# Performance work log

Measured on AMD Instinct MI355X. Metric: run time of the kernel, lower is better.

The kernel has to match this reference:

```python
import jax, jax.numpy as jnp
import numpy as np

D_EV, D_RGB, D_FUSED, D_REASON = 128, 128, 384, 384
D_INNER, D_STATE, D_CONV, DT_RANK = 2 * D_REASON, 16, 4, (D_REASON + 15) // 16
B, L = 4, 1024
LN_EPS = 1e-5


def setup_inputs() -> dict:
    key = jax.random.key(0)
    ks = jax.random.split(key, 16)
    s = lambda k, shp, scale=0.02: jax.random.normal(k, shp, jnp.float32) * scale
    inp = {
        "ev_tok": jax.random.normal(ks[0], (B, L, D_EV), jnp.float32),
        "rgb_tok": jax.random.normal(ks[1], (B, L, D_RGB), jnp.float32),
        "W_ev": s(ks[2], (D_EV, D_FUSED // 2)), "b_ev": jnp.zeros((D_FUSED // 2,), jnp.float32),
        "W_rgb": s(ks[3], (D_RGB, D_FUSED // 2)), "b_rgb": jnp.zeros((D_FUSED // 2,), jnp.float32),
        "ln_g": jnp.ones((D_FUSED,), jnp.float32), "ln_b": jnp.zeros((D_FUSED,), jnp.float32),
        "W_proj": s(ks[4], (D_FUSED, D_REASON)), "b_proj": jnp.zeros((D_REASON,), jnp.float32),
        "W_in": s(ks[5], (D_REASON, 2 * D_INNER)),
        "conv_w": s(ks[6], (D_INNER, 1, D_CONV), 0.1), "conv_b": jnp.zeros((D_INNER,), jnp.float32),
        "W_x": s(ks[7], (D_INNER, DT_RANK + 2 * D_STATE)),
        "W_dt": s(ks[8], (DT_RANK, D_INNER), 0.1), "b_dt": s(ks[9], (D_INNER,), 0.1),
        "A_log": jnp.tile(jnp.log(jnp.arange(1, D_STATE + 1, dtype=jnp.float32)), (D_INNER, 1)),
        "D_skip": jnp.ones((D_INNER,), jnp.float32),
        "W_out": s(ks[10], (D_INNER, D_REASON)),
    }
    return inp


def _selective_scan(u, delta, A, Bm, Cm, D_skip):
    # u, delta: [B,L,d]; Bm, Cm: [B,L,n]; A: [d,n]; D_skip: [d]
    deltaA = jnp.exp(delta[..., None] * A)                       # [B,L,d,n]
    deltaBu = delta[..., None] * Bm[:, :, None, :] * u[..., None]  # [B,L,d,n]

    def step(h, inp):
        dA, dBu, C_t = inp
        h = dA * h + dBu                                         # [B,d,n]
        y = jnp.einsum('bdn,bn->bd', h, C_t)
        return h, y

    h0 = jnp.zeros((u.shape[0], A.shape[0], A.shape[1]), u.dtype)
    xs = (jnp.moveaxis(deltaA, 1, 0), jnp.moveaxis(deltaBu, 1, 0), jnp.moveaxis(Cm, 1, 0))
    _, ys = jax.lax.scan(step, h0, xs)                           # [L,B,d]
    return jnp.moveaxis(ys, 0, 1) + u * D_skip


def _mamba_block(x, W_in, conv_w, conv_b, W_x, W_dt, b_dt, A_log, D_skip, W_out):
    xr = x @ W_in                                                # [B,L,2*d_inner]
    u, res = jnp.split(xr, 2, axis=-1)
    # causal depthwise conv over time
    uc = jnp.swapaxes(u, 1, 2)                                   # [B,d_inner,L]
    uc = jax.lax.conv_general_dilated(uc, conv_w, (1,), [(D_CONV - 1, 0)],
                                      dimension_numbers=('NCH', 'OIH', 'NCH'),
                                      feature_group_count=D_INNER)
    u = jax.nn.silu(jnp.swapaxes(uc, 1, 2) + conv_b)             # [B,L,d_inner]
    x_dbl = u @ W_x                                              # [B,L,dt_rank+2n]
    dt, Bm, Cm = jnp.split(x_dbl, [DT_RANK, DT_RANK + D_STATE], axis=-1)
    delta = jax.nn.softplus(dt @ W_dt + b_dt)                    # [B,L,d_inner]
    A = -jnp.exp(A_log)                                          # [d_inner,n]
    y = _selective_scan(u, delta, A, Bm, Cm, D_skip)
    y = y * jax.nn.silu(res)
    return y @ W_out


def reference(ev_tok, rgb_tok, W_ev, b_ev, W_rgb, b_rgb, ln_g, ln_b, W_proj, b_proj,
              W_in, conv_w, conv_b, W_x, W_dt, b_dt, A_log, D_skip, W_out):
    x = jnp.concatenate([ev_tok @ W_ev + b_ev, rgb_tok @ W_rgb + b_rgb], axis=-1)
    mu = jnp.mean(x, axis=-1, keepdims=True)
    var = jnp.mean(jnp.square(x - mu), axis=-1, keepdims=True)
    x = (x - mu) * jax.lax.rsqrt(var + LN_EPS) * ln_g + ln_b
    x = x @ W_proj + b_proj                                      # [B,L,d_reason]
    return _mamba_block(x, W_in, conv_w, conv_b, W_x, W_dt, b_dt, A_log, D_skip, W_out)
```

## Files before the change

### kernel.cpp

```cpp
#include <hip/hip_runtime.h>
#include <cstddef>
#include <cstdint>

#define L_SEQ 1024
#define NCHUNK 64
#define CLEN 16

typedef __bf16 bf16x8 __attribute__((ext_vector_type(8)));
typedef float f32x4 __attribute__((ext_vector_type(4)));

__device__ __forceinline__ float silu_f(float x) {
    return x / (1.f + __expf(-x));
}
__device__ __forceinline__ float exp2_fast(float x) { return exp2f(x); }

__device__ __forceinline__ unsigned short f2bf(float x) {
    union { float f; unsigned int u; } v; v.f = x;
    unsigned int r = (v.u + 0x7fffu + ((v.u >> 16) & 1u)) >> 16;
    return (unsigned short)r;
}
__device__ __forceinline__ float bf2f(unsigned short h) {
    union { float f; unsigned int u; } v; v.u = ((unsigned int)h) << 16;
    return v.f;
}
__device__ __forceinline__ unsigned int packf(float x) {
    unsigned short h = f2bf(x);
    unsigned short l = f2bf(x - bf2f(h));
    return ((unsigned int)h << 16) | (unsigned int)l;
}
__device__ __forceinline__ float unpackf(unsigned int pk) {
    return bf2f((unsigned short)(pk >> 16)) + bf2f((unsigned short)(pk & 0xffffu));
}

template<bool APK, int EPI, int SPLITS>
__global__ __launch_bounds__(256)
void gemm_bf3(const unsigned short* __restrict__ Ahi,
              const unsigned short* __restrict__ Alo,
              const unsigned int* __restrict__ Apk, int lda,
              const unsigned short* __restrict__ Bthi,
              const unsigned short* __restrict__ Btlo,
              const float* __restrict__ bias,
              float* __restrict__ Cf, float* __restrict__ Cf2,
              unsigned short* __restrict__ Chi, unsigned short* __restrict__ Clo,
              int Ks, int Ktot, int Nw)
{
    __shared__ unsigned short As[2][128][40];
    __shared__ unsigned short Bs[2][128][40];
    const int tid = threadIdx.x;
    const int lane = tid & 63;
    const int wave = tid >> 6;
    const int wm = wave >> 1, wn = wave & 1;

    const int gx = gridDim.x;
    const int nwg = gx * gridDim.y;
    const int lin = blockIdx.y * gx + blockIdx.x;
    const int swz = ((nwg & 7) == 0) ? ((lin & 7) * (nwg >> 3) + (lin >> 3)) : lin;
    const int m0 = (swz / gx) * 128, n0 = (swz % gx) * 128;
    const int z = (SPLITS > 1) ? blockIdx.z : 0;
    const int kbeg = z * Ks;

    const int srow = tid >> 1, sko = (tid & 1) * 16;

    f32x4 acc[4][4];
    #pragma unroll
    for (int i = 0; i < 4; ++i)
        #pragma unroll
        for (int j = 0; j < 4; ++j) {
            f32x4 zz = {0.f, 0.f, 0.f, 0.f};
            acc[i][j] = zz;
        }

    const size_t aoff = (size_t)(m0 + srow) * lda + sko;
    const size_t boff = (size_t)(n0 + srow) * Ktot + sko;

    uint4 ra[4], rb[4];

    auto load_regs = [&](int k0) {
        if constexpr (APK) {
            const unsigned int* ap = Apk + aoff + k0;
            ra[0] = *(const uint4*)(ap);
            ra[1] = *(const uint4*)(ap + 4);
            ra[2] = *(const uint4*)(ap + 8);
            ra[3] = *(const uint4*)(ap + 12);
        } else {
            ra[0] = *(const uint4*)(Ahi + aoff + k0);
            ra[1] = *(const uint4*)(Ahi + aoff + k0 + 8);
            ra[2] = *(const uint4*)(Alo + aoff + k0);
            ra[3] = *(const uint4*)(Alo + aoff + k0 + 8);
        }
        rb[0] = *(const uint4*)(Bthi + boff + k0);
        rb[1] = *(const uint4*)(Bthi + boff + k0 + 8);
        rb[2] = *(const uint4*)(Btlo + boff + k0);
        rb[3] = *(const uint4*)(Btlo + boff + k0 + 8);
    };

    auto store_lds = [&]() {
        uint4 h0, h1, l0, l1;
        if constexpr (APK) {
            uint4 p0 = ra[0], p1 = ra[1], p2 = ra[2], p3 = ra[3];
            h0.x = (p0.x >> 16) | (p0.y & 0xffff0000u);
            h0.y = (p0.z >> 16) | (p0.w & 0xffff0000u);
            h0.z = (p1.x >> 16) | (p1.y & 0xffff0000u);
            h0.w = (p1.z >> 16) | (p1.w & 0xffff0000u);
            h1.x = (p2.x >> 16) | (p2.y & 0xffff0000u);
            h1.y = (p2.z >> 16) | (p2.w & 0xffff0000u);
            h1.z = (p3.x >> 16) | (p3.y & 0xffff0000u);
            h1.w = (p3.z >> 16) | (p3.w & 0xffff0000u);
            l0.x = (p0.x & 0xffffu) | (p0.y << 16);
            l0.y = (p0.z & 0xffffu) | (p0.w << 16);
            l0.z = (p1.x & 0xffffu) | (p1.y << 16);
            l0.w = (p1.z & 0xffffu) | (p1.w << 16);
            l1.x = (p2.x & 0xffffu) | (p2.y << 16);
            l1.y = (p2.z & 0xffffu) | (p2.w << 16);
            l1.z = (p3.x & 0xffffu) | (p3.y << 16);
            l1.w = (p3.z & 0xffffu) | (p3.w << 16);
        } else {
            h0 = ra[0]; h1 = ra[1]; l0 = ra[2]; l1 = ra[3];
        }
        *(uint4*)&As[0][srow][sko]     = h0;
        *(uint4*)&As[0][srow][sko + 8] = h1;
        *(uint4*)&As[1][srow][sko]     = l0;
        *(uint4*)&As[1][srow][sko + 8] = l1;
        *(uint4*)&Bs[0][srow][sko]     = rb[0];
        *(uint4*)&Bs[0][srow][sko + 8] = rb[1];
        *(uint4*)&Bs[1][srow][sko]     = rb[2];
        *(uint4*)&Bs[1][srow][sko + 8] = rb[3];
    };

    const int fr = lane & 15, kq = lane >> 4;
    const int kend = kbeg + Ks;

    load_regs(kbeg);
    for (int k0 = kbeg; k0 < kend; k0 += 32) {
        store_lds();
        __syncthreads();
        if (k0 + 32 < kend) load_regs(k0 + 32);
        {
            bf16x8 aH[4], aL[4];
            #pragma unroll
            for (int i = 0; i < 4; ++i) {
                aH[i] = *(const bf16x8*)&As[0][wm * 64 + i * 16 + fr][kq * 8];
                aL[i] = *(const bf16x8*)&As[1][wm * 64 + i * 16 + fr][kq * 8];
            }
            #pragma unroll
            for (int j = 0; j < 4; ++j) {
                bf16x8 bH = *(const bf16x8*)&Bs[0][wn * 64 + j * 16 + fr][kq * 8];
                bf16x8 bL = *(const bf16x8*)&Bs[1][wn * 64 + j * 16 + fr][kq * 8];
                #pragma unroll
                for (int i = 0; i < 4; ++i)
                    acc[i][j] = __builtin_amdgcn_mfma_f32_16x16x32_bf16(aH[i], bH, acc[i][j], 0, 0, 0);
                #pragma unroll
                for (int i = 0; i < 4; ++i)
                    acc[i][j] = __builtin_amdgcn_mfma_f32_16x16x32_bf16(aL[i], bH, acc[i][j], 0, 0, 0);
                #pragma unroll
                for (int i = 0; i < 4; ++i)
                    acc[i][j] = __builtin_amdgcn_mfma_f32_16x16x32_bf16(aH[i], bL, acc[i][j], 0, 0, 0);
            }
        }
        __syncthreads();
    }

    float* myP = nullptr;
    if constexpr (EPI == 3) {
        float* base = (2 * z >= SPLITS) ? Cf2 : Cf;
        int sub = z - ((2 * z >= SPLITS) ? SPLITS / 2 : 0);
        myP = base + (size_t)sub * (size_t)(gridDim.y * 128) * Nw;
    }
    const int col = lane & 15, rq = lane >> 4;
    #pragma unroll
    for (int j = 0; j < 4; ++j) {
        int nn = n0 + wn * 64 + j * 16 + col;
        float bv = 0.f;
        if constexpr (EPI == 1 || EPI == 4) { if (bias) bv = bias[nn]; }
        #pragma unroll
        for (int i = 0; i < 4; ++i) {
            int mb = m0 + wm * 64 + i * 16 + rq * 4;
            #pragma unroll
            for (int r = 0; r < 4; ++r) {
                float o = acc[i][j][r] + bv;
                if constexpr (EPI == 1) {
                    unsigned short h = f2bf(o);
                    Chi[(size_t)(mb + r) * Nw + nn] = h;
                    Clo[(size_t)(mb + r) * Nw + nn] = f2bf(o - bf2f(h));
                } else if constexpr (EPI == 3) {
                    if (nn < Nw) myP[(size_t)(mb + r) * Nw + nn] = o;
                } else if constexpr (EPI == 4) {
                    if (nn < 768) Cf[(size_t)(mb + r) * 768 + nn] = o;
                    else          Cf2[(size_t)(mb + r) * 768 + (nn - 768)] = o;
                }
            }
        }
    }
}

__device__ __forceinline__ void wcvt_body(const float* __restrict__ W,
                                          unsigned short* __restrict__ Thi,
                                          unsigned short* __restrict__ Tlo,
                                          int K, int N, int nx, int local, int tid,
                                          float* t )
{
    const int n0 = (local % nx) * 32, k0 = (local / nx) * 32;
    const int r = tid >> 3, c4 = (tid & 7) * 4;
    float4 v = *(const float4*)(W + (size_t)(k0 + r) * N + n0 + c4);
    t[r * 33 + c4 + 0] = v.x; t[r * 33 + c4 + 1] = v.y;
    t[r * 33 + c4 + 2] = v.z; t[r * 33 + c4 + 3] = v.w;
    __syncthreads();
    unsigned short hs[4], ls[4];
    #pragma unroll
    for (int j = 0; j < 4; ++j) {
        float x = t[(c4 + j) * 33 + r];
        hs[j] = f2bf(x);
        ls[j] = f2bf(x - bf2f(hs[j]));
    }
    size_t o = (size_t)(n0 + r) * K + k0 + c4;
    uint2 hv, lv;
    hv.x = (unsigned)hs[0] | ((unsigned)hs[1] << 16);
    hv.y = (unsigned)hs[2] | ((unsigned)hs[3] << 16);
    lv.x = (unsigned)ls[0] | ((unsigned)ls[1] << 16);
    lv.y = (unsigned)ls[2] | ((unsigned)ls[3] << 16);
    *(uint2*)(Thi + o) = hv;
    *(uint2*)(Tlo + o) = lv;
}

__global__ __launch_bounds__(256)
void prep_all(const float* __restrict__ W_proj, const float* __restrict__ W_in,
              const float* __restrict__ W_out, const float* __restrict__ W_x,
              const float* __restrict__ W_dt, const float* __restrict__ b_proj,
              const float* __restrict__ W_ev, const float* __restrict__ W_rgb,
              const float* __restrict__ b_ev, const float* __restrict__ b_rgb,
              const float* __restrict__ ev, const float* __restrict__ rgb,
              unsigned short* __restrict__ wtp_hi, unsigned short* __restrict__ wtp_lo,
              unsigned short* __restrict__ wti_hi, unsigned short* __restrict__ wti_lo,
              unsigned short* __restrict__ wto_hi, unsigned short* __restrict__ wto_lo,
              unsigned short* __restrict__ btc_hi, unsigned short* __restrict__ btc_lo,
              unsigned short* __restrict__ wct_hi, unsigned short* __restrict__ wct_lo,
              unsigned short* __restrict__ wpd_hi, unsigned short* __restrict__ wpd_lo,
              float* __restrict__ biascat, float* __restrict__ bias_pi,
              unsigned int* __restrict__ apk)
{
    __shared__ float t[32 * 33];
    const int blk = blockIdx.x;
    const int tid = threadIdx.x;
    if (blk < 144) {
        wcvt_body(W_proj, wtp_hi, wtp_lo, 384, 384, 12, blk, tid, t);
    } else if (blk < 720) {
        wcvt_body(W_in, wti_hi, wti_lo, 384, 1536, 48, blk - 144, tid, t);
    } else if (blk < 1008) {
        wcvt_body(W_out, wto_hi, wto_lo, 768, 384, 12, blk - 720, tid, t);
    } else if (blk < 1392) {
        const int flat = (blk - 1008) * 256 + tid;
        const int r = flat / 768, k = flat % 768;
        const int row = (r < 32) ? r : (768 + r);
        float val = (r < 32) ? W_x[(size_t)k * 56 + 24 + r] : 0.f;
        unsigned short h = f2bf(val);
        btc_hi[(size_t)row * 768 + k] = h;
        btc_lo[(size_t)row * 768 + k] = f2bf(val - bf2f(h));
    } else if (blk < 3696) {
        const int flat = (blk - 1392) * 256 + tid;
        const int j = flat / 768, k = flat % 768;
        const float* xp = W_x + (size_t)k * 56;
        float acc = 0.f;
        #pragma unroll
        for (int r = 0; r < 24; ++r)
            acc = fmaf(xp[r], W_dt[(size_t)r * 768 + j], acc);
        unsigned short h = f2bf(acc);
        btc_hi[(size_t)(32 + j) * 768 + k] = h;
        btc_lo[(size_t)(32 + j) * 768 + k] = f2bf(acc - bf2f(h));
    } else if (blk < 4082) {
        const int flat = (blk - 3696) * 256 + tid;
        if (flat < 384 * 256) {
            const int n = flat >> 8, k = flat & 255;
            float val = 0.f;
            if (n < 192) { if (k < 128) val = W_ev[(size_t)k * 192 + n]; }
            else         { if (k >= 128) val = W_rgb[(size_t)(k - 128) * 192 + (n - 192)]; }
            unsigned short h = f2bf(val);
            wct_hi[flat] = h;
            wct_lo[flat] = f2bf(val - bf2f(h));
        } else if (flat < 384 * 256 + 384) {
            const int i = flat - 384 * 256;
            biascat[i] = (i < 192) ? b_ev[i] : b_rgb[i - 192];
        }
    } else if (blk < 5106) {
        const int idx = (blk - 4082) * 1024 + tid * 4;
        const int m = idx >> 8, kk = idx & 255;
        #pragma unroll
        for (int q = 0; q < 4; ++q) {
            int k = kk + q;
            float val = (k < 128) ? ev[(size_t)m * 128 + k] : rgb[(size_t)m * 128 + k - 128];
            apk[(size_t)m * 256 + k] = packf(val);
        }
    } else if (blk < 5682) {
        const int flat = (blk - 5106) * 256 + tid;
        float val = W_proj[flat];
        unsigned short h = f2bf(val);
        wpd_hi[flat] = h;
        wpd_lo[flat] = f2bf(val - bf2f(h));
    } else {
        const int j = (blk - 5682) * 256 + tid;
        float acc = 0.f;
        for (int i = 0; i < 384; ++i)
            acc = fmaf(b_proj[i], W_in[(size_t)i * 1536 + j], acc);
        bias_pi[j] = acc;
    }
}

__global__ __launch_bounds__(256)
void ln2(const float* __restrict__ ep0, const float* __restrict__ ep1,
         const float* __restrict__ biascat,
         const float* __restrict__ g, const float* __restrict__ b,
         unsigned short* __restrict__ hi, unsigned short* __restrict__ lo)
{
    const int lane = threadIdx.x & 63;
    const int row = blockIdx.x * 4 + (threadIdx.x >> 6);
    const float* p0 = ep0 + (size_t)row * 384;
    const float* p1 = ep1 + (size_t)row * 384;
    unsigned short* ph = hi + (size_t)row * 384;
    unsigned short* pl = lo + (size_t)row * 384;
    float v[6];
    #pragma unroll
    for (int i = 0; i < 6; ++i) {
        int c = i * 64 + lane;
        v[i] = p0[c] + p1[c] + biascat[c];
    }
    float s = v[0] + v[1] + v[2] + v[3] + v[4] + v[5];
    #pragma unroll
    for (int m = 32; m >= 1; m >>= 1) s += __shfl_xor(s, m);
    const float mu = s * (1.f / 384.f);
    float q = 0.f;
    #pragma unroll
    for (int i = 0; i < 6; ++i) { float dv = v[i] - mu; q = fmaf(dv, dv, q); }
    #pragma unroll
    for (int m = 32; m >= 1; m >>= 1) q += __shfl_xor(q, m);
    const float inv = 1.f / sqrtf(q * (1.f / 384.f) + 1e-5f);
    #pragma unroll
    for (int i = 0; i < 6; ++i) {
        int c = i * 64 + lane;
        float o = (v[i] - mu) * inv * g[c] + b[c];
        unsigned short h = f2bf(o);
        ph[c] = h;
        pl[c] = f2bf(o - bf2f(h));
    }
}

__global__ __launch_bounds__(256)
void conv_pack(const float* __restrict__ u_pre, const float* __restrict__ conv_w,
               const float* __restrict__ conv_b, unsigned int* __restrict__ upk)
{
    const int d = blockIdx.x * 256 + threadIdx.x;
    const int t0 = blockIdx.z * L_SEQ + blockIdx.y * 16;
    const float w0 = conv_w[d * 4 + 0], w1 = conv_w[d * 4 + 1];
    const float w2 = conv_w[d * 4 + 2], w3 = conv_w[d * 4 + 3];
    const float cb = conv_b[d];
    const float* xp = u_pre + (size_t)t0 * 768 + d;
    float x1, x2, x3;
    if (blockIdx.y == 0) { x1 = x2 = x3 = 0.f; }
    else {
        x1 = xp[-1 * 768];
        x2 = xp[-2 * 768];
        x3 = xp[-3 * 768];
    }
    unsigned int* op = upk + (size_t)t0 * 768 + d;
    #pragma unroll 4
    for (int i = 0; i < 16; ++i) {
        float cur = xp[i * 768];
        float a = cb;
        a = fmaf(x3, w0, a);
        a = fmaf(x2, w1, a);
        a = fmaf(x1, w2, a);
        a = fmaf(cur, w3, a);
        op[i * 768] = packf(silu_f(a));
        x3 = x2; x2 = x1; x1 = cur;
    }
}

__global__ __launch_bounds__(256)
void combine_fused(const float* __restrict__ P0, const float* __restrict__ P1,
                   const float* __restrict__ b_dt,
                   float* __restrict__ bc, float* __restrict__ delta)
{
    const int g = blockIdx.x * 256 + threadIdx.x;
    const int m = g / 200, c0 = (g % 200) * 4;
    const float* a = P0 + (size_t)m * 800 + c0;
    const float* bb = P1 + (size_t)m * 800 + c0;
    float4 s0 = *(const float4*)a;
    float4 s1 = *(const float4*)bb;
    float sv[4] = {s0.x + s1.x, s0.y + s1.y, s0.z + s1.z, s0.w + s1.w};
    #pragma unroll
    for (int j = 0; j < 4; ++j) {
        int col = c0 + j;
        if (col < 32) {
            bc[(size_t)m * 32 + col] = sv[j];
        } else {
            float o = sv[j] + b_dt[col - 32];
            delta[(size_t)m * 768 + col - 32] = fmaxf(o, 0.f) + log1pf(expf(-fabsf(o)));
        }
    }
}

__global__ __launch_bounds__(256)
void combine_out(const float* __restrict__ PA, const float* __restrict__ PB,
                 float* __restrict__ out)
{
    const int g = blockIdx.x * 256 + threadIdx.x;
    const size_t o = (size_t)g * 4;
    float4 a0 = *(const float4*)(PA + o);
    float4 a1 = *(const float4*)(PA + 1572864 + o);
    float4 a2 = *(const float4*)(PB + o);
    float4 a3 = *(const float4*)(PB + 1572864 + o);
    float4 r;
    r.x = a0.x + a1.x + a2.x + a3.x;
    r.y = a0.y + a1.y + a2.y + a3.y;
    r.z = a0.z + a1.z + a2.z + a3.z;
    r.w = a0.w + a1.w + a2.w + a3.w;
    *(float4*)(out + o) = r;
}

__global__ __launch_bounds__(256)
void scan_a2(const float* __restrict__ delta, const unsigned int* __restrict__ upk,
             const float* __restrict__ bc, const float* __restrict__ A_log,
             float* __restrict__ dsum_out, float* __restrict__ Bc)
{
    __shared__ float Bsh[CLEN][16];
    const int tid = threadIdx.x;
    const int d = blockIdx.x * 256 + tid;
    const int c = blockIdx.y, b = blockIdx.z;
    const int row0 = b * L_SEQ + c * CLEN;
    {
        int t = tid >> 4, n = tid & 15;
        Bsh[t][n] = bc[(size_t)(row0 + t) * 32 + n];
    }
    float AL2[16];
    {
        const float* ap = A_log + d * 16;
        #pragma unroll
        for (int n = 0; n < 16; ++n)
            AL2[n] = -__expf(ap[n]) * 1.44269504f;
    }
    __syncthreads();
    float h[16];
    #pragma unroll
    for (int n = 0; n < 16; ++n) h[n] = 0.f;
    float dsum = 0.f;
    const float* dp = delta + (size_t)row0 * 768 + d;
    const unsigned int* up = upk + (size_t)row0 * 768 + d;
    #pragma unroll 4
    for (int t = 0; t < CLEN; ++t) {
        float dt = dp[t * 768];
        float ut = unpackf(up[t * 768]);
        float du = dt * ut;
        dsum += dt;
        #pragma unroll
        for (int n = 0; n < 16; ++n) {
            float dA = exp2_fast(dt * AL2[n]);
            h[n] = fmaf(dA, h[n], du * Bsh[t][n]);
        }
    }
    dsum_out[(size_t)(b * 768 + d) * NCHUNK + c] = dsum;
    float* bcp = Bc + (((size_t)(b * 768 + d)) * NCHUNK + c) * 16;
    #pragma unroll
    for (int n = 0; n < 16; ++n) bcp[n] = h[n];
}

__global__ __launch_bounds__(256)
void scan_b2(const float* __restrict__ dsum, const float* __restrict__ A_log,
             float* __restrict__ BcHin)
{
    const size_t flat = (size_t)blockIdx.x * 256 + threadIdx.x;
    const size_t bd = flat >> 4;
    const int n = (int)(flat & 15);
    const int d = (int)(bd % 768);
    const float AL2 = -__expf(A_log[d * 16 + n]) * 1.44269504f;
    const float* dsp = dsum + bd * NCHUNK;
    const size_t base = bd * (NCHUNK * 16) + n;
    float h = 0.f;
    for (int c = 0; c < NCHUNK; ++c) {
        size_t i = base + (size_t)c * 16;
        float a = exp2_fast(AL2 * dsp[c]);
        float bb = BcHin[i];
        BcHin[i] = h;
        h = fmaf(a, h, bb);
    }
}

__global__ __launch_bounds__(256)
void scan_c2(float* __restrict__ delta, const unsigned int* __restrict__ upk,
             const float* __restrict__ bc, const float* __restrict__ A_log,
             const float* __restrict__ Hin, const float* __restrict__ D_skip,
             const float* __restrict__ res)
{
    __shared__ float Bsh[CLEN][16];
    __shared__ float Csh[CLEN][16];
    const int tid = threadIdx.x;
    const int d = blockIdx.x * 256 + tid;
    const int c = blockIdx.y, b = blockIdx.z;
    const int row0 = b * L_SEQ + c * CLEN;
    {
        int t = tid >> 4, n = tid & 15;
        const float* xp = bc + (size_t)(row0 + t) * 32;
        Bsh[t][n] = xp[n];
        Csh[t][n] = xp[16 + n];
    }
    float AL2[16];
    {
        const float* ap = A_log + d * 16;
        #pragma unroll
        for (int n = 0; n < 16; ++n)
            AL2[n] = -__expf(ap[n]) * 1.44269504f;
    }
    float h[16];
    {
        const float* hp = Hin + (((size_t)(b * 768 + d)) * NCHUNK + c) * 16;
        #pragma unroll
        for (int n = 0; n < 16; ++n) h[n] = hp[n];
    }
    const float Ds = D_skip[d];
    __syncthreads();
    float* dp = delta + (size_t)row0 * 768 + d;
    const unsigned int* up = upk + (size_t)row0 * 768 + d;
    const float* rp = res + (size_t)row0 * 768 + d;
    #pragma unroll 4
    for (int t = 0; t < CLEN; ++t) {
        float dt = dp[t * 768];
        float ut = unpackf(up[t * 768]);
        float du = dt * ut;
        float y = 0.f;
        #pragma unroll
        for (int n = 0; n < 16; ++n) {
            float dA = exp2_fast(dt * AL2[n]);
            h[n] = fmaf(dA, h[n], du * Bsh[t][n]);
            y = fmaf(h[n], Csh[t][n], y);
        }
        float rr = rp[t * 768];
        float gy = fmaf(ut, Ds, y) * silu_f(rr);
        dp[t * 768] = __builtin_bit_cast(float, packf(gy));
    }
}

extern "C" void kernel_launch(void* const* d_in, const int* in_sizes, int n_in,
                              void* d_out, int out_size, void* d_ws, size_t ws_size,
                              hipStream_t stream)
{
    const float* ev     = (const float*)d_in[0];
    const float* rgb    = (const float*)d_in[1];
    const float* W_ev   = (const float*)d_in[2];
    const float* b_ev   = (const float*)d_in[3];
    const float* W_rgb  = (const float*)d_in[4];
    const float* b_rgb  = (const float*)d_in[5];
    const float* ln_g   = (const float*)d_in[6];
    const float* ln_b   = (const float*)d_in[7];
    const float* W_proj = (const float*)d_in[8];
    const float* b_proj = (const float*)d_in[9];
    const float* W_in   = (const float*)d_in[10];
    const float* conv_w = (const float*)d_in[11];
    const float* conv_b = (const float*)d_in[12];
    const float* W_x    = (const float*)d_in[13];
    const float* W_dt   = (const float*)d_in[14];
    const float* b_dt   = (const float*)d_in[15];
    const float* A_log  = (const float*)d_in[16];
    const float* D_skip = (const float*)d_in[17];
    const float* W_out  = (const float*)d_in[18];
    float* out = (float*)d_out;

    float* ws = (float*)d_ws;
    const size_t O0 = 0;
    const size_t O1 = 3145728;
    const size_t O2 = 6422528;
    const size_t O3 = 9568256;
    const size_t O4 = 12713984;
    const size_t O5 = 16056320;

    float* res   = ws + O0;
    unsigned int* apk = (unsigned int*)(ws + O0);
    float* u_pre = ws + O1;
    float* ep0   = ws + O1;
    float* ep1   = ws + O1 + 1572864;
    float* P0    = ws + O1;
    float* outPA = ws + O1;
    unsigned int* upk = (unsigned int*)(ws + O2);
    unsigned short* xfh = (unsigned short*)(ws + O2);
    unsigned short* xfl = xfh + 1572864;
    unsigned short* wpi_hi = (unsigned short*)(ws + O2 + 1572864);
    unsigned short* wpi_lo = wpi_hi + 589824;
    float* delta = ws + O3;
    unsigned short* wtp_hi = (unsigned short*)(ws + O3);
    unsigned short* wtp_lo = wtp_hi + 147456;
    unsigned short* wpd_hi = wtp_lo + 147456;
    unsigned short* wpd_lo = wpd_hi + 147456;
    unsigned short* wti_hi = wpd_lo + 147456;
    unsigned short* wti_lo = wti_hi + 589824;
    unsigned short* btc_hi = (unsigned short*)(ws + O3 + 884736);
    unsigned short* btc_lo = btc_hi + 688128;
    float* P1    = ws + O4;
    float* dsum  = ws + O4;
    float* BcHin = ws + O4 + 196608;
    float* outPB = ws + O4;
    unsigned short* wct_hi = (unsigned short*)(ws + O5);
    unsigned short* wct_lo = wct_hi + 98304;
    float* biascat = ws + O5 + 98304;
    float* bias_pi = ws + O5 + 98688;
    unsigned short* wto_hi = (unsigned short*)(ws + O5 + 100224);
    unsigned short* wto_lo = wto_hi + 589824;
    float* bc    = ws + O5 + 690048;

    dim3 blk(256);

    prep_all<<<5688, blk, 0, stream>>>(
        W_proj, W_in, W_out, W_x, W_dt, b_proj, W_ev, W_rgb, b_ev, b_rgb, ev, rgb,
        wtp_hi, wtp_lo, wti_hi, wti_lo, wto_hi, wto_lo,
        btc_hi, btc_lo, wct_hi, wct_lo, wpd_hi, wpd_lo, biascat, bias_pi, apk);

    gemm_bf3<true, 3, 2><<<dim3(3, 32, 2), blk, 0, stream>>>(
        nullptr, nullptr, apk, 256, wct_hi, wct_lo, nullptr,
        ep0, ep1, nullptr, nullptr, 128, 256, 384);
    gemm_bf3<false, 1, 1><<<dim3(3, 12), blk, 0, stream>>>(
        wti_hi, wti_lo, nullptr, 384, wpd_hi, wpd_lo, nullptr,
        nullptr, nullptr, wpi_hi, wpi_lo, 384, 384, 384);
    ln2<<<1024, blk, 0, stream>>>(ep0, ep1, biascat, ln_g, ln_b, xfh, xfl);
    gemm_bf3<false, 4, 1><<<dim3(12, 32), blk, 0, stream>>>(
        xfh, xfl, nullptr, 384, wpi_hi, wpi_lo, bias_pi,
        u_pre, res, nullptr, nullptr, 384, 384, 1536);
    conv_pack<<<dim3(3, 64, 4), blk, 0, stream>>>(u_pre, conv_w, conv_b, upk);
    gemm_bf3<true, 3, 2><<<dim3(7, 32, 2), blk, 0, stream>>>(
        nullptr, nullptr, upk, 768, btc_hi, btc_lo, nullptr,
        P0, P1, nullptr, nullptr, 384, 768, 800);
    combine_fused<<<3200, blk, 0, stream>>>(P0, P1, b_dt, bc, delta);
    scan_a2<<<dim3(3, NCHUNK, 4), blk, 0, stream>>>(delta, upk, bc, A_log, dsum, BcHin);
    scan_b2<<<192, blk, 0, stream>>>(dsum, A_log, BcHin);
    scan_c2<<<dim3(3, NCHUNK, 4), blk, 0, stream>>>(delta, upk, bc, A_log, BcHin, D_skip, res);
    gemm_bf3<true, 3, 4><<<dim3(3, 32, 4), blk, 0, stream>>>(
        nullptr, nullptr, (const unsigned int*)delta, 768, wto_hi, wto_lo, nullptr,
        outPA, outPB, nullptr, nullptr, 192, 768, 384);
    combine_out<<<1536, blk, 0, stream>>>(outPA, outPB, out);
}
```

Baseline: 269.6 us.

## Load GEMM MFMA fragments directly from global memory, removing LDS staging

The bf16x3 GEMM kernel no longer stages A and B tiles through shared memory with register prefetch and barriers. Each wave now loads its MFMA operand fragments straight from global memory, with per-row offsets computed once, and unpacks packed A in registers. This removes LDS traffic and both __syncthreads per k-step. In exchange, the two waves sharing a tile row or column each load the same data, redundant global/L2 traffic rises, and there is no software prefetch left to hide load latency.

```diff
diff --git a/kernel.cpp b/kernel.cpp
--- a/kernel.cpp
+++ b/kernel.cpp
@@ -30,6 +30,9 @@
 }
 __device__ __forceinline__ float unpackf(unsigned int pk) {
     return bf2f((unsigned short)(pk >> 16)) + bf2f((unsigned short)(pk & 0xffffu));
+}
+__device__ __forceinline__ bf16x8 u4_to_bf8(uint4 u) {
+    return __builtin_bit_cast(bf16x8, u);
 }
 
 template<bool APK, int EPI, int SPLITS>
@@ -44,8 +47,6 @@
               unsigned short* __restrict__ Chi, unsigned short* __restrict__ Clo,
               int Ks, int Ktot, int Nw)
 {
-    __shared__ unsigned short As[2][128][40];
-    __shared__ unsigned short Bs[2][128][40];
     const int tid = threadIdx.x;
     const int lane = tid & 63;
     const int wave = tid >> 6;
@@ -58,8 +59,19 @@
     const int m0 = (swz / gx) * 128, n0 = (swz % gx) * 128;
     const int z = (SPLITS > 1) ? blockIdx.z : 0;
     const int kbeg = z * Ks;
-
-    const int srow = tid >> 1, sko = (tid & 1) * 16;
+    const int kend = kbeg + Ks;
+
+    const int fr = lane & 15;
+    const int kq8 = (lane >> 4) * 8;
+    const int mbw = m0 + wm * 64, nbw = n0 + wn * 64;
+
+    unsigned int aoffs[4], boffs[4];
+    #pragma unroll
+    for (int i = 0; i < 4; ++i)
+        aoffs[i] = (unsigned int)(mbw + i * 16 + fr) * (unsigned int)lda + kq8;
+    #pragma unroll
+    for (int j = 0; j < 4; ++j)
+        boffs[j] = (unsigned int)(nbw + j * 16 + fr) * (unsigned int)Ktot + kq8;
 
     f32x4 acc[4][4];
     #pragma unroll
@@ -70,94 +82,47 @@
             acc[i][j] = zz;
         }
 
-    const size_t aoff = (size_t)(m0 + srow) * lda + sko;
-    const size_t boff = (size_t)(n0 + srow) * Ktot + sko;
-
-    uint4 ra[4], rb[4];
-
-    auto load_regs = [&](int k0) {
+    for (int k0 = kbeg; k0 < kend; k0 += 32) {
+        bf16x8 aH[4], aL[4];
         if constexpr (APK) {
-            const unsigned int* ap = Apk + aoff + k0;
-            ra[0] = *(const uint4*)(ap);
-            ra[1] = *(const uint4*)(ap + 4);
-            ra[2] = *(const uint4*)(ap + 8);
-            ra[3] = *(const uint4*)(ap + 12);
-        } else {
-            ra[0] = *(const uint4*)(Ahi + aoff + k0);
-            ra[1] = *(const uint4*)(Ahi + aoff + k0 + 8);
-            ra[2] = *(const uint4*)(Alo + aoff + k0);
-            ra[3] = *(const uint4*)(Alo + aoff + k0 + 8);
-        }
-        rb[0] = *(const uint4*)(Bthi + boff + k0);
-        rb[1] = *(const uint4*)(Bthi + boff + k0 + 8);
-        rb[2] = *(const uint4*)(Btlo + boff + k0);
-        rb[3] = *(const uint4*)(Btlo + boff + k0 + 8);
-    };
-
-    auto store_lds = [&]() {
-        uint4 h0, h1, l0, l1;
-        if constexpr (APK) {
-            uint4 p0 = ra[0], p1 = ra[1], p2 = ra[2], p3 = ra[3];
-            h0.x = (p0.x >> 16) | (p0.y & 0xffff0000u);
-            h0.y = (p0.z >> 16) | (p0.w & 0xffff0000u);
-            h0.z = (p1.x >> 16) | (p1.y & 0xffff0000u);
-            h0.w = (p1.z >> 16) | (p1.w & 0xffff0000u);
-            h1.x = (p2.x >> 16) | (p2.y & 0xffff0000u);
-            h1.y = (p2.z >> 16) | (p2.w & 0xffff0000u);
-            h1.z = (p3.x >> 16) | (p3.y & 0xffff0000u);
-            h1.w = (p3.z >> 16) | (p3.w & 0xffff0000u);
-            l0.x = (p0.x & 0xffffu) | (p0.y << 16);
-            l0.y = (p0.z & 0xffffu) | (p0.w << 16);
-            l0.z = (p1.x & 0xffffu) | (p1.y << 16);
-            l0.w = (p1.z & 0xffffu) | (p1.w << 16);
-            l1.x = (p2.x & 0xffffu) | (p2.y << 16);
-            l1.y = (p2.z & 0xffffu) | (p2.w << 16);
-            l1.z = (p3.x & 0xffffu) | (p3.y << 16);
-            l1.w = (p3.z & 0xffffu) | (p3.w << 16);
-        } else {
-            h0 = ra[0]; h1 = ra[1]; l0 = ra[2]; l1 = ra[3];
-        }
-        *(uint4*)&As[0][srow][sko]     = h0;
-        *(uint4*)&As[0][srow][sko + 8] = h1;
-        *(uint4*)&As[1][srow][sko]     = l0;
-        *(uint4*)&As[1][srow][sko + 8] = l1;
-        *(uint4*)&Bs[0][srow][sko]     = rb[0];
-        *(uint4*)&Bs[0][srow][sko + 8] = rb[1];
-        *(uint4*)&Bs[1][srow][sko]     = rb[2];
-        *(uint4*)&Bs[1][srow][sko + 8] = rb[3];
-    };
-
-    const int fr = lane & 15, kq = lane >> 4;
-    const int kend = kbeg + Ks;
-
-    load_regs(kbeg);
-    for (int k0 = kbeg; k0 < kend; k0 += 32) {
-        store_lds();
-        __syncthreads();
-        if (k0 + 32 < kend) load_regs(k0 + 32);
-        {
-            bf16x8 aH[4], aL[4];
             #pragma unroll
             for (int i = 0; i < 4; ++i) {
-                aH[i] = *(const bf16x8*)&As[0][wm * 64 + i * 16 + fr][kq * 8];
-                aL[i] = *(const bf16x8*)&As[1][wm * 64 + i * 16 + fr][kq * 8];
+                const unsigned int* p = Apk + aoffs[i] + k0;
+                uint4 p0 = *(const uint4*)p;
+                uint4 p1 = *(const uint4*)(p + 4);
+                uint4 h, l;
+                h.x = (p0.x >> 16) | (p0.y & 0xffff0000u);
+                h.y = (p0.z >> 16) | (p0.w & 0xffff0000u);
+                h.z = (p1.x >> 16) | (p1.y & 0xffff0000u);
+                h.w = (p1.z >> 16) | (p1.w & 0xffff0000u);
+                l.x = (p0.x & 0xffffu) | (p0.y << 16);
+                l.y = (p0.z & 0xffffu) | (p0.w << 16);
+                l.z = (p1.x & 0xffffu) | (p1.y << 16);
+                l.w = (p1.z & 0xffffu) | (p1.w << 16);
+                aH[i] = u4_to_bf8(h);
+                aL[i] = u4_to_bf8(l);
             }
+        } else {
             #pragma unroll
-            for (int j = 0; j < 4; ++j) {
-                bf16x8 bH = *(const bf16x8*)&Bs[0][wn * 64 + j * 16 + fr][kq * 8];
-                bf16x8 bL = *(const bf16x8*)&Bs[1][wn * 64 + j * 16 + fr][kq * 8];
-                #pragma unroll
-                for (int i = 0; i < 4; ++i)
-                    acc[i][j] = __builtin_amdgcn_mfma_f32_16x16x32_bf16(aH[i], bH, acc[i][j], 0, 0, 0);
-                #pragma unroll
-                for (int i = 0; i < 4; ++i)
-                    acc[i][j] = __builtin_amdgcn_mfma_f32_16x16x32_bf16(aL[i], bH, acc[i][j], 0, 0, 0);
-                #pragma unroll
-                for (int i = 0; i < 4; ++i)
-                    acc[i][j] = __builtin_amdgcn_mfma_f32_16x16x32_bf16(aH[i], bL, acc[i][j], 0, 0, 0);
+            for (int i = 0; i < 4; ++i) {
+                aH[i] = *(const bf16x8*)(Ahi + aoffs[i] + k0);
+                aL[i] = *(const bf16x8*)(Alo + aoffs[i] + k0);
             }
         }
-        __syncthreads();
+        #pragma unroll
+        for (int j = 0; j < 4; ++j) {
+            bf16x8 bH = *(const bf16x8*)(Bthi + boffs[j] + k0);
+            bf16x8 bL = *(const bf16x8*)(Btlo + boffs[j] + k0);
+            #pragma unroll
+            for (int i = 0; i < 4; ++i)
+                acc[i][j] = __builtin_amdgcn_mfma_f32_16x16x32_bf16(aH[i], bH, acc[i][j], 0, 0, 0);
+            #pragma unroll
+            for (int i = 0; i < 4; ++i)
+                acc[i][j] = __builtin_amdgcn_mfma_f32_16x16x32_bf16(aL[i], bH, acc[i][j], 0, 0, 0);
+            #pragma unroll
+            for (int i = 0; i < 4; ++i)
+                acc[i][j] = __builtin_amdgcn_mfma_f32_16x16x32_bf16(aH[i], bL, acc[i][j], 0, 0, 0);
+        }
     }
 
     float* myP = nullptr;
```

After: 298.5 us. +10.7%, slower.

## Unfold the W_x·W_dt product into a low-rank two-stage delta projection

Applied to the files above, without the earlier changes.

Previously the precomputed W_x·W_dt product (768x768) was folded into one wide GEMM that produced delta and B/C together. Now u is multiplied by the narrow W_x (56 cols, 8-way split-K), a combine kernel reduces the partials and packs the dt-rank part, and a small K=32 GEMM applies W_dt with bias and softplus fused into its epilogue. This cuts GEMM FLOPs and removes the costly weight-product precompute and the unused W_proj transpose from prep, at the cost of an extra launch and a split-K reduction pass.

```diff
diff --git a/kernel.cpp b/kernel.cpp
--- a/kernel.cpp
+++ b/kernel.cpp
@@ -171,7 +171,7 @@
     for (int j = 0; j < 4; ++j) {
         int nn = n0 + wn * 64 + j * 16 + col;
         float bv = 0.f;
-        if constexpr (EPI == 1 || EPI == 4) { if (bias) bv = bias[nn]; }
+        if constexpr (EPI == 1 || EPI == 4 || EPI == 6) { if (bias) bv = bias[nn]; }
         #pragma unroll
         for (int i = 0; i < 4; ++i) {
             int mb = m0 + wm * 64 + i * 16 + rq * 4;
@@ -187,6 +187,9 @@
                 } else if constexpr (EPI == 4) {
                     if (nn < 768) Cf[(size_t)(mb + r) * 768 + nn] = o;
                     else          Cf2[(size_t)(mb + r) * 768 + (nn - 768)] = o;
+                } else if constexpr (EPI == 6) {
+                    float sp = fmaxf(o, 0.f) + log1pf(expf(-fabsf(o)));
+                    Cf[(size_t)(mb + r) * Nw + nn] = sp;
                 }
             }
         }
@@ -223,51 +226,30 @@
 }
 
 __global__ __launch_bounds__(256)
-void prep_all(const float* __restrict__ W_proj, const float* __restrict__ W_in,
-              const float* __restrict__ W_out, const float* __restrict__ W_x,
-              const float* __restrict__ W_dt, const float* __restrict__ b_proj,
+void prep_all(const float* __restrict__ W_in, const float* __restrict__ W_out,
+              const float* __restrict__ W_x, const float* __restrict__ W_dt,
+              const float* __restrict__ W_proj, const float* __restrict__ b_proj,
               const float* __restrict__ W_ev, const float* __restrict__ W_rgb,
               const float* __restrict__ b_ev, const float* __restrict__ b_rgb,
               const float* __restrict__ ev, const float* __restrict__ rgb,
-              unsigned short* __restrict__ wtp_hi, unsigned short* __restrict__ wtp_lo,
               unsigned short* __restrict__ wti_hi, unsigned short* __restrict__ wti_lo,
               unsigned short* __restrict__ wto_hi, unsigned short* __restrict__ wto_lo,
-              unsigned short* __restrict__ btc_hi, unsigned short* __restrict__ btc_lo,
               unsigned short* __restrict__ wct_hi, unsigned short* __restrict__ wct_lo,
               unsigned short* __restrict__ wpd_hi, unsigned short* __restrict__ wpd_lo,
+              unsigned short* __restrict__ wx56t_hi, unsigned short* __restrict__ wx56t_lo,
+              unsigned short* __restrict__ wdtT_hi, unsigned short* __restrict__ wdtT_lo,
               float* __restrict__ biascat, float* __restrict__ bias_pi,
               unsigned int* __restrict__ apk)
 {
     __shared__ float t[32 * 33];
     const int blk = blockIdx.x;
     const int tid = threadIdx.x;
-    if (blk < 144) {
-        wcvt_body(W_proj, wtp_hi, wtp_lo, 384, 384, 12, blk, tid, t);
-    } else if (blk < 720) {
-        wcvt_body(W_in, wti_hi, wti_lo, 384, 1536, 48, blk - 144, tid, t);
-    } else if (blk < 1008) {
-        wcvt_body(W_out, wto_hi, wto_lo, 768, 384, 12, blk - 720, tid, t);
-    } else if (blk < 1392) {
-        const int flat = (blk - 1008) * 256 + tid;
-        const int r = flat / 768, k = flat % 768;
-        const int row = (r < 32) ? r : (768 + r);
-        float val = (r < 32) ? W_x[(size_t)k * 56 + 24 + r] : 0.f;
-        unsigned short h = f2bf(val);
-        btc_hi[(size_t)row * 768 + k] = h;
-        btc_lo[(size_t)row * 768 + k] = f2bf(val - bf2f(h));
-    } else if (blk < 3696) {
-        const int flat = (blk - 1392) * 256 + tid;
-        const int j = flat / 768, k = flat % 768;
-        const float* xp = W_x + (size_t)k * 56;
-        float acc = 0.f;
-        #pragma unroll
-        for (int r = 0; r < 24; ++r)
-            acc = fmaf(xp[r], W_dt[(size_t)r * 768 + j], acc);
-        unsigned short h = f2bf(acc);
-        btc_hi[(size_t)(32 + j) * 768 + k] = h;
-        btc_lo[(size_t)(32 + j) * 768 + k] = f2bf(acc - bf2f(h));
-    } else if (blk < 4082) {
-        const int flat = (blk - 3696) * 256 + tid;
+    if (blk < 576) {
+        wcvt_body(W_in, wti_hi, wti_lo, 384, 1536, 48, blk, tid, t);
+    } else if (blk < 864) {
+        wcvt_body(W_out, wto_hi, wto_lo, 768, 384, 12, blk - 576, tid, t);
+    } else if (blk < 1250) {
+        const int flat = (blk - 864) * 256 + tid;
         if (flat < 384 * 256) {
             const int n = flat >> 8, k = flat & 255;
             float val = 0.f;
@@ -280,8 +262,8 @@
             const int i = flat - 384 * 256;
             biascat[i] = (i < 192) ? b_ev[i] : b_rgb[i - 192];
         }
-    } else if (blk < 5106) {
-        const int idx = (blk - 4082) * 1024 + tid * 4;
+    } else if (blk < 2274) {
+        const int idx = (blk - 1250) * 1024 + tid * 4;
         const int m = idx >> 8, kk = idx & 255;
         #pragma unroll
         for (int q = 0; q < 4; ++q) {
@@ -289,18 +271,32 @@
             float val = (k < 128) ? ev[(size_t)m * 128 + k] : rgb[(size_t)m * 128 + k - 128];
             apk[(size_t)m * 256 + k] = packf(val);
         }
-    } else if (blk < 5682) {
-        const int flat = (blk - 5106) * 256 + tid;
+    } else if (blk < 2850) {
+        const int flat = (blk - 2274) * 256 + tid;
         float val = W_proj[flat];
         unsigned short h = f2bf(val);
         wpd_hi[flat] = h;
         wpd_lo[flat] = f2bf(val - bf2f(h));
-    } else {
-        const int j = (blk - 5682) * 256 + tid;
+    } else if (blk < 2856) {
+        const int j = (blk - 2850) * 256 + tid;
         float acc = 0.f;
         for (int i = 0; i < 384; ++i)
             acc = fmaf(b_proj[i], W_in[(size_t)i * 1536 + j], acc);
         bias_pi[j] = acc;
+    } else if (blk < 3240) {
+        const int flat = (blk - 2856) * 256 + tid;
+        const int r = flat / 768, k = flat % 768;
+        float val = (r < 56) ? W_x[(size_t)k * 56 + r] : 0.f;
+        unsigned short h = f2bf(val);
+        wx56t_hi[(size_t)r * 768 + k] = h;
+        wx56t_lo[(size_t)r * 768 + k] = f2bf(val - bf2f(h));
+    } else {
+        const int flat = (blk - 3240) * 256 + tid;
+        const int j = flat >> 5, kk = flat & 31;
+        float val = (kk < 24) ? W_dt[(size_t)kk * 768 + j] : 0.f;
+        unsigned short h = f2bf(val);
+        wdtT_hi[(size_t)j * 32 + kk] = h;
+        wdtT_lo[(size_t)j * 32 + kk] = f2bf(val - bf2f(h));
     }
 }
 
@@ -374,26 +370,20 @@
 }
 
 __global__ __launch_bounds__(256)
-void combine_fused(const float* __restrict__ P0, const float* __restrict__ P1,
-                   const float* __restrict__ b_dt,
-                   float* __restrict__ bc, float* __restrict__ delta)
+void combine1(const float* __restrict__ P, unsigned int* __restrict__ dtpk,
+              float* __restrict__ bc)
 {
     const int g = blockIdx.x * 256 + threadIdx.x;
-    const int m = g / 200, c0 = (g % 200) * 4;
-    const float* a = P0 + (size_t)m * 800 + c0;
-    const float* bb = P1 + (size_t)m * 800 + c0;
-    float4 s0 = *(const float4*)a;
-    float4 s1 = *(const float4*)bb;
-    float sv[4] = {s0.x + s1.x, s0.y + s1.y, s0.z + s1.z, s0.w + s1.w};
-    #pragma unroll
-    for (int j = 0; j < 4; ++j) {
-        int col = c0 + j;
-        if (col < 32) {
-            bc[(size_t)m * 32 + col] = sv[j];
-        } else {
-            float o = sv[j] + b_dt[col - 32];
-            delta[(size_t)m * 768 + col - 32] = fmaxf(o, 0.f) + log1pf(expf(-fabsf(o)));
-        }
+    const int m = g >> 6, c = g & 63;
+    float s = 0.f;
+    #pragma unroll
+    for (int z = 0; z < 8; ++z)
+        s += P[(size_t)z * 262144 + (size_t)m * 64 + c];
+    if (c < 24) {
+        dtpk[(size_t)m * 32 + c] = packf(s);
+    } else {
+        if (c < 32) dtpk[(size_t)m * 32 + c] = 0u;
+        if (c < 56) bc[(size_t)m * 32 + (c - 24)] = s;
     }
 }
 
@@ -571,10 +561,10 @@
 
     float* res   = ws + O0;
     unsigned int* apk = (unsigned int*)(ws + O0);
-    float* u_pre = ws + O1;
     float* ep0   = ws + O1;
     float* ep1   = ws + O1 + 1572864;
-    float* P0    = ws + O1;
+    float* u_pre = ws + O1;
+    unsigned int* dtpk = (unsigned int*)(ws + O1);
     float* outPA = ws + O1;
     unsigned int* upk = (unsigned int*)(ws + O2);
     unsigned short* xfh = (unsigned short*)(ws + O2);
@@ -582,15 +572,11 @@
     unsigned short* wpi_hi = (unsigned short*)(ws + O2 + 1572864);
     unsigned short* wpi_lo = wpi_hi + 589824;
     float* delta = ws + O3;
-    unsigned short* wtp_hi = (unsigned short*)(ws + O3);
-    unsigned short* wtp_lo = wtp_hi + 147456;
-    unsigned short* wpd_hi = wtp_lo + 147456;
+    unsigned short* wti_hi = (unsigned short*)(ws + O3);
+    unsigned short* wti_lo = wti_hi + 589824;
+    unsigned short* wpd_hi = (unsigned short*)(ws + O3 + 589824);
     unsigned short* wpd_lo = wpd_hi + 147456;
-    unsigned short* wti_hi = wpd_lo + 147456;
-    unsigned short* wti_lo = wti_hi + 589824;
-    unsigned short* btc_hi = (unsigned short*)(ws + O3 + 884736);
-    unsigned short* btc_lo = btc_hi + 688128;
-    float* P1    = ws + O4;
+    float* Pz    = ws + O4;
     float* dsum  = ws + O4;
     float* BcHin = ws + O4 + 196608;
     float* outPB = ws + O4;
@@ -599,15 +585,19 @@
     float* biascat = ws + O5 + 98304;
     float* bias_pi = ws + O5 + 98688;
     unsigned short* wto_hi = (unsigned short*)(ws + O5 + 100224);
-    unsigned short* wto_lo = wto_hi + 589824;
-    float* bc    = ws + O5 + 690048;
+    unsigned short* wto_lo = wto_hi + 294912;
+    float* bc    = ws + O5 + 395136;
+    unsigned short* wx56t_hi = (unsigned short*)(ws + O5 + 526208);
+    unsigned short* wx56t_lo = wx56t_hi + 98304;
+    unsigned short* wdtT_hi = (unsigned short*)(ws + O5 + 624512);
+    unsigned short* wdtT_lo = wdtT_hi + 24576;
 
     dim3 blk(256);
 
-    prep_all<<<5688, blk, 0, stream>>>(
-        W_proj, W_in, W_out, W_x, W_dt, b_proj, W_ev, W_rgb, b_ev, b_rgb, ev, rgb,
-        wtp_hi, wtp_lo, wti_hi, wti_lo, wto_hi, wto_lo,
-        btc_hi, btc_lo, wct_hi, wct_lo, wpd_hi, wpd_lo, biascat, bias_pi, apk);
+    prep_all<<<3336, blk, 0, stream>>>(
+        W_in, W_out, W_x, W_dt, W_proj, b_proj, W_ev, W_rgb, b_ev, b_rgb, ev, rgb,
+        wti_hi, wti_lo, wto_hi, wto_lo, wct_hi, wct_lo, wpd_hi, wpd_lo,
+        wx56t_hi, wx56t_lo, wdtT_hi, wdtT_lo, biascat, bias_pi, apk);
 
     gemm_bf3<true, 3, 2><<<dim3(3, 32, 2), blk, 0, stream>>>(
         nullptr, nullptr, apk, 256, wct_hi, wct_lo, nullptr,
@@ -620,10 +610,13 @@
         xfh, xfl, nullptr, 384, wpi_hi, wpi_lo, bias_pi,
         u_pre, res, nullptr, nullptr, 384, 384, 1536);
     conv_pack<<<dim3(3, 64, 4), blk, 0, stream>>>(u_pre, conv_w, conv_b, upk);
-    gemm_bf3<true, 3, 2><<<dim3(7, 32, 2), blk, 0, stream>>>(
-        nullptr, nullptr, upk, 768, btc_hi, btc_lo, nullptr,
-        P0, P1, nullptr, nullptr, 384, 768, 800);
-    combine_fused<<<3200, blk, 0, stream>>>(P0, P1, b_dt, bc, delta);
+    gemm_bf3<true, 3, 8><<<dim3(1, 32, 8), blk, 0, stream>>>(
+        nullptr, nullptr, upk, 768, wx56t_hi, wx56t_lo, nullptr,
+        Pz, Pz + 1048576, nullptr, nullptr, 96, 768, 64);
+    combine1<<<1024, blk, 0, stream>>>(Pz, dtpk, bc);
+    gemm_bf3<true, 6, 1><<<dim3(6, 32), blk, 0, stream>>>(
+        nullptr, nullptr, dtpk, 32, wdtT_hi, wdtT_lo, b_dt,
+        delta, nullptr, nullptr, nullptr, 32, 32, 768);
     scan_a2<<<dim3(3, NCHUNK, 4), blk, 0, stream>>>(delta, upk, bc, A_log, dsum, BcHin);
     scan_b2<<<192, blk, 0, stream>>>(dsum, A_log, BcHin);
     scan_c2<<<dim3(3, NCHUNK, 4), blk, 0, stream>>>(delta, upk, bc, A_log, BcHin, D_skip, res);
```

Result: faster. 245.0 us (-9.1%).
